# Kernel tuning notes

Measured on AMD Instinct MI355X. Metric: run time of the kernel, lower is better.

The kernel has to match this reference:

```python
import jax, jax.numpy as jnp
import numpy as np

S = 4096      # total packed sequence length (8 images x 512 patches)
D = 1152      # hidden_dim
H = 16        # num_heads
HD = D // H   # head_dim = 72
MLPD = 4304   # mlp_dim
EPS = 1e-5


def setup_inputs() -> dict:
    key = jax.random.key(0)
    ks = jax.random.split(key, 16)
    f32 = jnp.float32
    w = lambda k, shp: (jax.random.normal(k, shp, f32) * 0.02)
    hidden_states = jax.random.normal(ks[0], (S, D), f32)
    cu_seqlens = (jnp.arange(9, dtype=jnp.int32) * (S // 8))  # [0,512,...,4096]
    angles = jax.random.uniform(ks[1], (S, HD // 2), f32, 0.0, 2.0 * np.pi)
    rope_cos = jnp.cos(angles)
    rope_sin = jnp.sin(angles)
    return {
        "hidden_states": hidden_states,
        "cu_seqlens": cu_seqlens,
        "rope_cos": rope_cos,
        "rope_sin": rope_sin,
        "norm0_scale": jnp.ones((D,), f32),
        "norm0_bias": jnp.zeros((D,), f32),
        "wqkv_w": w(ks[2], (D, 3 * D)),
        "wqkv_b": jnp.zeros((3 * D,), f32),
        "wo_w": w(ks[3], (D, D)),
        "wo_b": jnp.zeros((D,), f32),
        "norm1_scale": jnp.ones((D,), f32),
        "norm1_bias": jnp.zeros((D,), f32),
        "fc0_w": w(ks[4], (D, MLPD)),
        "fc0_b": jnp.zeros((MLPD,), f32),
        "fc1_w": w(ks[5], (MLPD, D)),
        "fc1_b": jnp.zeros((D,), f32),
    }


def _layernorm(x, scale, bias):
    m = jnp.mean(x, axis=-1, keepdims=True)
    v = jnp.mean(jnp.square(x - m), axis=-1, keepdims=True)
    return (x - m) * jax.lax.rsqrt(v + EPS) * scale + bias


def _rope(x, cos, sin):
    # x: (S, H, HD). Complex multiply (x0 + i x1) * (cos + i sin) in real form.
    xr = x.reshape(S, H, HD // 2, 2)
    x0, x1 = xr[..., 0], xr[..., 1]
    c = cos[:, None, :]  # (S, 1, HD/2) broadcast over heads
    s = sin[:, None, :]
    o0 = x0 * c - x1 * s
    o1 = x0 * s + x1 * c
    return jnp.stack([o0, o1], axis=-1).reshape(S, H, HD)


def _block_diag_bias(cu_seqlens):
    positions = jnp.arange(S)
    starts, ends = cu_seqlens[:-1], cu_seqlens[1:]
    in_seg = (positions[:, None] >= starts[None, :]) & (positions[:, None] < ends[None, :])
    seg = jnp.argmax(in_seg.astype(jnp.int32), axis=-1)  # (S,)
    same = seg[:, None] == seg[None, :]
    return jnp.where(same, 0.0, jnp.finfo(jnp.float32).min)  # (S, S)


def reference(hidden_states, cu_seqlens, rope_cos, rope_sin,
              norm0_scale, norm0_bias, wqkv_w, wqkv_b, wo_w, wo_b,
              norm1_scale, norm1_bias, fc0_w, fc0_b, fc1_w, fc1_b):
    # pre-norm attention block
    x = _layernorm(hidden_states, norm0_scale, norm0_bias)
    qkv = (x @ wqkv_w + wqkv_b).reshape(S, 3, H, HD)
    q, k, v = qkv[:, 0], qkv[:, 1], qkv[:, 2]
    q = _rope(q, rope_cos, rope_sin)
    k = _rope(k, rope_cos, rope_sin)
    bias = _block_diag_bias(cu_seqlens)  # (S, S)
    scale = HD ** -0.5
    scores = jnp.einsum('shd,thd->hst', q, k) * scale + bias[None, :, :]
    probs = jax.nn.softmax(scores, axis=-1)
    attn = jnp.einsum('hst,thd->shd', probs, v).reshape(S, D)
    attn = attn @ wo_w + wo_b
    h = hidden_states + attn
    # pre-norm MLP block
    y = _layernorm(h, norm1_scale, norm1_bias)
    y = jax.nn.gelu(y @ fc0_w + fc0_b) @ fc1_w + fc1_b
    return h + y
```

## Files before the change

kernel.cpp:

```cpp
#include <hip/hip_runtime.h>


#define DEV __device__ __forceinline__

typedef __attribute__((ext_vector_type(8))) short short8;
typedef __attribute__((ext_vector_type(4))) float f32x4;

typedef const void __attribute__((address_space(1))) gvoid;
typedef void __attribute__((address_space(3))) lvoid;

DEV ushort f2bf(float f) {
  union { float f; unsigned u; } x; x.f = f;
  unsigned r = (x.u + 0x7FFFu + ((x.u >> 16) & 1u)) >> 16;
  return (ushort)r;
}

DEV float bf2f(ushort u) {
  union { unsigned u; float f; } x; x.u = (unsigned)u << 16;
  return x.f;
}

DEV void gload_lds16(const void* g, void* l) {
  __builtin_amdgcn_global_load_lds((gvoid*)g, (lvoid*)l, 16, 0, 0);
}

DEV f32x4 mfma16(short8 a, short8 b, f32x4 c) {
  return __builtin_amdgcn_mfma_f32_16x16x32_bf16(a, b, c, 0, 0, 0);
}

DEV float gelu_tanh(float x) {
  float x3 = x * x * x;
  return 0.5f * x * (1.f + tanhf(0.7978845608f * (x + 0.044715f * x3)));
}

__global__ void wconv_t(const float* __restrict__ src, ushort* __restrict__ dst,
                        int K, int N, int NP, int KP) {
  __shared__ float tile[32][33];
  const int k0 = blockIdx.x * 32, n0 = blockIdx.y * 32;
  const int tx = threadIdx.x & 31, ty = threadIdx.x >> 5;
#pragma unroll
  for (int i = 0; i < 4; ++i) {
    int r = ty + i * 8;
    float v = 0.f;
    if (k0 + r < K && n0 + tx < N) v = src[(size_t)(k0 + r) * N + n0 + tx];
    tile[tx][r] = v;
  }
  __syncthreads();
#pragma unroll
  for (int i = 0; i < 4; ++i) {
    int r = ty + i * 8;
    dst[(size_t)(n0 + r) * KP + k0 + tx] = f2bf(tile[r][tx]);
  }
}

__global__ __launch_bounds__(256) void ln_bf16(const float* __restrict__ x,
                                               const float* __restrict__ sc,
                                               const float* __restrict__ bi,
                                               ushort* __restrict__ out) {
  const int row = blockIdx.x, tid = threadIdx.x;
  const float* xr = x + (size_t)row * 1152;
  const int n = (tid < 128) ? 5 : 4;
  float vals[5];
  float s = 0.f, s2 = 0.f;
#pragma unroll
  for (int i = 0; i < 5; ++i) {
    if (i < n) { float v = xr[tid + i * 256]; vals[i] = v; s += v; s2 += v * v; }
  }
#pragma unroll
  for (int off = 32; off; off >>= 1) { s += __shfl_xor(s, off); s2 += __shfl_xor(s2, off); }
  __shared__ float rs[4], rs2[4];
  if ((tid & 63) == 0) { rs[tid >> 6] = s; rs2[tid >> 6] = s2; }
  __syncthreads();
  s = rs[0] + rs[1] + rs[2] + rs[3];
  s2 = rs2[0] + rs2[1] + rs2[2] + rs2[3];
  const float mean = s * (1.f / 1152.f);
  const float var = s2 * (1.f / 1152.f) - mean * mean;
  const float rstd = rsqrtf(var + 1e-5f);
  ushort* orow = out + (size_t)row * 1152;
  for (int i = 0; i < n; ++i) {
    int c = tid + i * 256;
    orow[c] = f2bf((vals[i] - mean) * rstd * sc[c] + bi[c]);
  }
}

template <int EPI>
__global__ __launch_bounds__(512, 2) void gemm_p(
    const ushort* __restrict__ A, const ushort* __restrict__ Bt,
    const float* __restrict__ bias, const float* __restrict__ resid,
    float* __restrict__ outf, ushort* __restrict__ outh,
    int N, int Kstride, int NT, int n_valid) {
  __shared__ ushort L[3][24576];
  const int tid = threadIdx.x;
  const int lane = tid & 63, wave = tid >> 6;
  const int l15 = lane & 15, lg = lane >> 4;

  const int nx = gridDim.x, ny = gridDim.y;
  const int nwg = nx * ny * gridDim.z;
  int flat = (blockIdx.z * ny + blockIdx.y) * nx + blockIdx.x;
  flat = (flat & 7) * (nwg >> 3) + (flat >> 3);
  const int bx = flat % nx;
  const int rem = flat / nx;
  const int by = rem % ny;
  const int bz = rem / ny;
  const int m0 = by * 256, n0 = bx * 128;
  const int k0 = bz * NT * 64;

  const int swz = ((tid & 7) ^ ((tid >> 3) & 7)) * 8;
  const int rstg = tid >> 3;
  const ushort* Ag = A + (size_t)(m0 + rstg) * Kstride + k0 + swz;
  const ushort* Bg = Bt + (size_t)(n0 + rstg) * Kstride + k0 + swz;

  auto stage = [&](int b, int t) {
    ushort* d = &L[b][0];
#pragma unroll
    for (int i = 0; i < 4; ++i)
      gload_lds16(Ag + ((size_t)i * 64) * Kstride + t * 64,
                  d + (i * 512 + wave * 64) * 8);
#pragma unroll
    for (int i = 0; i < 2; ++i)
      gload_lds16(Bg + ((size_t)i * 64) * Kstride + t * 64,
                  d + 16384 + (i * 512 + wave * 64) * 8);
  };

  const int wm = (wave >> 1) * 64, wn = (wave & 1) * 64;
  const int cph0 = (lg ^ (l15 & 7)) * 8;
  const int cph1 = ((4 + lg) ^ (l15 & 7)) * 8;

  auto rdfrag = [&](int b, short8 (&fa)[4][2], short8 (&fb)[4][2]) {
    const ushort* la = &L[b][0];
    const ushort* lb = &L[b][16384];
#pragma unroll
    for (int mf = 0; mf < 4; ++mf) {
      fa[mf][0] = *(const short8*)&la[(wm + mf * 16 + l15) * 64 + cph0];
      fa[mf][1] = *(const short8*)&la[(wm + mf * 16 + l15) * 64 + cph1];
    }
#pragma unroll
    for (int nf = 0; nf < 4; ++nf) {
      fb[nf][0] = *(const short8*)&lb[(wn + nf * 16 + l15) * 64 + cph0];
      fb[nf][1] = *(const short8*)&lb[(wn + nf * 16 + l15) * 64 + cph1];
    }
  };

  f32x4 acc[4][4] = {};
  short8 fa[2][4][2], fb[2][4][2];

  stage(0, 0); stage(1, 1); stage(2, 2);
  asm volatile("s_waitcnt vmcnt(6)" ::: "memory");
  __builtin_amdgcn_s_barrier();
  rdfrag(0, fa[0], fb[0]);

  int b0 = 0, b1 = 1;

#define GBODY(TT, CUR, NXT)                                                   \
  {                                                                           \
    const int _t = (TT);                                                      \
    if (_t + 1 < NT) rdfrag(b1, fa[NXT], fb[NXT]);                            \
    if (_t + 3 < NT) stage(b0, _t + 3);                                       \
    __builtin_amdgcn_s_setprio(1);                                            \
    _Pragma("unroll") for (int mf = 0; mf < 4; ++mf)                          \
      _Pragma("unroll") for (int nf = 0; nf < 4; ++nf) {                      \
        acc[mf][nf] = mfma16(fa[CUR][mf][0], fb[CUR][nf][0], acc[mf][nf]);    \
        acc[mf][nf] = mfma16(fa[CUR][mf][1], fb[CUR][nf][1], acc[mf][nf]);    \
      }                                                                       \
    __builtin_amdgcn_s_setprio(0);                                            \
    asm volatile("s_waitcnt lgkmcnt(0)" ::: "memory");                        \
    __builtin_amdgcn_sched_barrier(0);                                        \
    if (_t + 3 < NT) { asm volatile("s_waitcnt vmcnt(6)" ::: "memory"); }     \
    else if (_t + 2 < NT) { asm volatile("s_waitcnt vmcnt(0)" ::: "memory"); }\
    if (_t + 1 < NT) __builtin_amdgcn_s_barrier();                            \
    const int _b2 = 3 - b0 - b1; b0 = b1; b1 = _b2;                           \
  }

  for (int t = 0; t < NT; t += 2) {
    GBODY(t, 0, 1);
    GBODY(t + 1, 1, 0);
  }
#undef GBODY

  float* outp = outf;
  if constexpr (EPI == 0) outp = outf + (size_t)bz * ((size_t)4096 * N);
  const int cb = n0 + wn + l15;
  const int rb = m0 + wm + lg * 4;
#pragma unroll
  for (int j = 0; j < 4; ++j) {
    const int col = cb + j * 16;
    const float bv = (EPI != 0 && col < n_valid) ? bias[col] : 0.f;
#pragma unroll
    for (int i = 0; i < 4; ++i) {
#pragma unroll
      for (int r = 0; r < 4; ++r) {
        const int row = rb + i * 16 + r;
        const size_t idx = (size_t)row * N + col;
        const float v = acc[i][j][r] + bv;
        if constexpr (EPI == 0) outp[idx] = v;
        else if constexpr (EPI == 1) outf[idx] = resid[idx] + v;
        else if constexpr (EPI == 2) outh[idx] = f2bf(gelu_tanh(v));
        else outh[idx] = f2bf(v);
      }
    }
  }
}

__global__ __launch_bounds__(256) void ksum_reduce(
    const float* __restrict__ hb, const float* __restrict__ bias,
    const float* __restrict__ p0, const float* __restrict__ p1,
    float* __restrict__ out) {
  const f32x4* hb4 = (const f32x4*)hb;
  const f32x4* b4 = (const f32x4*)bias;
  const f32x4* p04 = (const f32x4*)p0;
  const f32x4* p14 = (const f32x4*)p1;
  f32x4* o4 = (f32x4*)out;
  const int total = 4096 * 288;
  for (int i = blockIdx.x * 256 + threadIdx.x; i < total; i += gridDim.x * 256) {
    f32x4 r = hb4[i] + b4[i % 288] + p04[i] + p14[i];
    o4[i] = r;
  }
}

__global__ void rope_pack(const ushort* __restrict__ qkv,
                          const float* __restrict__ cosp, const float* __restrict__ sinp,
                          ushort* __restrict__ qp, ushort* __restrict__ kp) {
  const int t = blockIdx.x * 256 + threadIdx.x;
  const int d = t % 96;
  const int hs = t / 96;
  const int h = hs & 15;
  const int s = hs >> 4;
  const size_t dst = ((size_t)h * 4096 + s) * 96 + d;
  if (d >= 72) { qp[dst] = 0; kp[dst] = 0; return; }
  const int i = d >> 1;
  const float c = cosp[s * 36 + i], sn = sinp[s * 36 + i];
  const size_t base = (size_t)s * 3456 + h * 72;
  const float q0 = bf2f(qkv[base + (d & ~1)]), q1 = bf2f(qkv[base + (d | 1)]);
  const float k0 = bf2f(qkv[base + 1152 + (d & ~1)]), k1 = bf2f(qkv[base + 1152 + (d | 1)]);
  float qo, ko;
  if ((d & 1) == 0) { qo = q0 * c - q1 * sn; ko = k0 * c - k1 * sn; }
  else              { qo = q0 * sn + q1 * c; ko = k0 * sn + k1 * c; }
  qp[dst] = f2bf(qo * 0.1178511302f);
  kp[dst] = f2bf(ko);
}

__global__ void v_pack(const ushort* __restrict__ qkv, ushort* __restrict__ vt) {
  __shared__ ushort lv[96][64];
  const int b = blockIdx.x;
  const int h = b >> 6;
  const int s0 = (b & 63) << 6;
  const int tid = threadIdx.x;
#pragma unroll
  for (int it = 0; it < 24; ++it) {
    int idx = tid + it * 256;
    int d = idx % 96, sl = idx / 96;
    lv[d][sl] = (d < 72) ? qkv[(size_t)(s0 + sl) * 3456 + 2304 + h * 72 + d] : (ushort)0;
  }
  __syncthreads();
#pragma unroll
  for (int it = 0; it < 24; ++it) {
    int idx = tid + it * 256;
    int d = idx >> 6, sl = idx & 63;
    vt[((size_t)h * 96 + d) * 4096 + s0 + sl] = lv[d][sl];
  }
}

__global__ __launch_bounds__(256) void attn_kernel(
    const ushort* __restrict__ qp, const ushort* __restrict__ kp,
    const ushort* __restrict__ vt, ushort* __restrict__ attn_out) {
  __shared__ ushort lp[4][16 * 32];
  const int tid = threadIdx.x, lane = tid & 63, wave = tid >> 6;
  const int l15 = lane & 15, lg = lane >> 4;
  const int b = blockIdx.x;
  const int h = b >> 6;
  const int rem = b & 63;
  const int seg = rem >> 3, qt = rem & 7;
  const int q0 = seg * 512 + qt * 64 + wave * 16;

  short8 aq[3];
  const ushort* qrow = qp + ((size_t)h * 4096 + q0 + l15) * 96 + lg * 8;
  aq[0] = *(const short8*)(qrow);
  aq[1] = *(const short8*)(qrow + 32);
  aq[2] = *(const short8*)(qrow + 64);

  f32x4 oacc[5] = {};
  float mrow[4] = {-1e30f, -1e30f, -1e30f, -1e30f};
  float srow[4] = {0.f, 0.f, 0.f, 0.f};

  const ushort* kbase = kp + ((size_t)h * 4096 + seg * 512) * 96;
  const ushort* vbase = vt + (size_t)h * 96 * 4096 + seg * 512;
  ushort* lpw = lp[wave];

  for (int kc = 0; kc < 16; ++kc) {
    f32x4 sc[2] = {};
#pragma unroll
    for (int n = 0; n < 2; ++n) {
      const ushort* krow = kbase + (size_t)(kc * 32 + n * 16 + l15) * 96 + lg * 8;
#pragma unroll
      for (int c = 0; c < 3; ++c) {
        short8 kb = *(const short8*)(krow + c * 32);
        sc[n] = mfma16(aq[c], kb, sc[n]);
      }
    }
    float corr[4];
#pragma unroll
    for (int j = 0; j < 4; ++j) {
      float v = fmaxf(sc[0][j], sc[1][j]);
      v = fmaxf(v, __shfl_xor(v, 1));
      v = fmaxf(v, __shfl_xor(v, 2));
      v = fmaxf(v, __shfl_xor(v, 4));
      v = fmaxf(v, __shfl_xor(v, 8));
      float mn = fmaxf(mrow[j], v);
      corr[j] = __expf(mrow[j] - mn);
      mrow[j] = mn;
    }
    float p0[4], p1[4];
#pragma unroll
    for (int j = 0; j < 4; ++j) {
      p0[j] = __expf(sc[0][j] - mrow[j]);
      p1[j] = __expf(sc[1][j] - mrow[j]);
      float ps = p0[j] + p1[j];
      ps += __shfl_xor(ps, 1);
      ps += __shfl_xor(ps, 2);
      ps += __shfl_xor(ps, 4);
      ps += __shfl_xor(ps, 8);
      srow[j] = srow[j] * corr[j] + ps;
    }
#pragma unroll
    for (int n = 0; n < 5; ++n)
#pragma unroll
      for (int j = 0; j < 4; ++j)
        oacc[n][j] *= corr[j];
#pragma unroll
    for (int j = 0; j < 4; ++j) {
      int row = lg * 4 + j;
      lpw[row * 32 + l15] = f2bf(p0[j]);
      lpw[row * 32 + 16 + l15] = f2bf(p1[j]);
    }
    __syncthreads();
    short8 pa = *(const short8*)&lpw[l15 * 32 + lg * 8];
    const ushort* vrow = vbase + kc * 32 + lg * 8;
#pragma unroll
    for (int n = 0; n < 5; ++n) {
      short8 vb = *(const short8*)(vrow + (size_t)(n * 16 + l15) * 4096);
      oacc[n] = mfma16(pa, vb, oacc[n]);
    }
    __syncthreads();
  }
#pragma unroll
  for (int j = 0; j < 4; ++j) {
    float inv = 1.f / srow[j];
    int row = q0 + lg * 4 + j;
#pragma unroll
    for (int n = 0; n < 5; ++n) {
      int col = n * 16 + l15;
      if (col < 72)
        attn_out[(size_t)row * 1152 + h * 72 + col] = f2bf(oacc[n][j] * inv);
    }
  }
}

extern "C" void kernel_launch(void* const* d_in, const int* in_sizes, int n_in,
                              void* d_out, int out_size, void* d_ws, size_t ws_size,
                              hipStream_t stream) {
  (void)in_sizes; (void)n_in; (void)out_size;
  const float* hidden = (const float*)d_in[0];
  const float* ropec = (const float*)d_in[2];
  const float* ropes = (const float*)d_in[3];
  const float* n0s = (const float*)d_in[4];
  const float* n0b = (const float*)d_in[5];
  const float* wqkv = (const float*)d_in[6];
  const float* bqkv = (const float*)d_in[7];
  const float* wo = (const float*)d_in[8];
  const float* bo = (const float*)d_in[9];
  const float* n1s = (const float*)d_in[10];
  const float* n1b = (const float*)d_in[11];
  const float* wfc0 = (const float*)d_in[12];
  const float* bfc0 = (const float*)d_in[13];
  const float* wfc1 = (const float*)d_in[14];
  const float* bfc1 = (const float*)d_in[15];
  float* out = (float*)d_out;

  char* ws = (char*)d_ws;
  ushort* x_bf   = (ushort*)(ws + 0);
  ushort* wqkv_t = (ushort*)(ws + 9437184);
  ushort* wo_t   = (ushort*)(ws + 17399808);
  ushort* fc0_t  = (ushort*)(ws + 20054016);
  ushort* fc1_t  = (ushort*)(ws + 30081024);
  ushort* qkv_bf = (ushort*)(ws + 40108032);
  ushort* mid    = (ushort*)(ws + 40108032);
  ushort* q_pad  = (ushort*)(ws + 96731136);
  ushort* k_pad  = (ushort*)(ws + 109314048);
  ushort* vt     = (ushort*)(ws + 121896960);
  float*  pbuf   = (float*)(ws + 96731136);
  ushort* attn   = (ushort*)(ws + 134479872);
  float*  hbuf   = (float*)(ws + 143917056);
  ushort* yln    = (ushort*)(ws + 162791424);
  if (ws_size < 172228608) return;

  wconv_t<<<dim3(36, 108), 256, 0, stream>>>(wqkv, wqkv_t, 1152, 3456, 3456, 1152);
  wconv_t<<<dim3(36, 36), 256, 0, stream>>>(wo, wo_t, 1152, 1152, 1152, 1152);
  wconv_t<<<dim3(36, 136), 256, 0, stream>>>(wfc0, fc0_t, 1152, 4304, 4352, 1152);
  wconv_t<<<dim3(136, 36), 256, 0, stream>>>(wfc1, fc1_t, 4304, 1152, 1152, 4352);

  ln_bf16<<<4096, 256, 0, stream>>>(hidden, n0s, n0b, x_bf);

  gemm_p<3><<<dim3(27, 16), 512, 0, stream>>>(x_bf, wqkv_t, bqkv, nullptr, nullptr, qkv_bf,
                                              3456, 1152, 18, 3456);
  rope_pack<<<24576, 256, 0, stream>>>(qkv_bf, ropec, ropes, q_pad, k_pad);
  v_pack<<<1024, 256, 0, stream>>>(qkv_bf, vt);

  attn_kernel<<<1024, 256, 0, stream>>>(q_pad, k_pad, vt, attn);

  gemm_p<1><<<dim3(9, 16), 512, 0, stream>>>(attn, wo_t, bo, hidden, hbuf, nullptr,
                                             1152, 1152, 18, 1152);
  ln_bf16<<<4096, 256, 0, stream>>>(hbuf, n1s, n1b, yln);

  gemm_p<2><<<dim3(34, 16), 512, 0, stream>>>(yln, fc0_t, bfc0, nullptr, nullptr, mid,
                                              4352, 1152, 18, 4304);
  gemm_p<0><<<dim3(9, 16, 2), 512, 0, stream>>>(mid, fc1_t, nullptr, nullptr, pbuf, nullptr,
                                                1152, 4352, 34, 1152);
  ksum_reduce<<<2048, 256, 0, stream>>>(hbuf, bfc1, pbuf, pbuf + (size_t)4096 * 1152, out);
}
```

Before: 378.3 us.

## Use 256x256 GEMM tiles with fine-grained quarter-step pipeline and vectorize rope_pack

The GEMM kernel moves from 256x128 to 256x256 output tiles with double-buffered LDS. Each k-step is split into four MFMA quarters, interleaved with staged global-to-LDS loads and fragment reads under explicit barriers. Weight buffers are padded to multiples of 256 columns to fit the new tile width, and the grid dimensions and workspace layout are updated to match. rope_pack is also vectorized to process 8 elements per thread with 16-byte loads and stores. The larger tile halves B traffic per output, but it uses more accumulator registers and fewer workgroups, which hurts tile quantization on the 1152-wide GEMMs.

```diff
diff --git a/kernel.cpp b/kernel.cpp
--- a/kernel.cpp
+++ b/kernel.cpp
@@ -83,16 +83,36 @@
   }
 }
 
+#define BAR __builtin_amdgcn_s_barrier()
+#define LGKM0 do { asm volatile("s_waitcnt lgkmcnt(0)" ::: "memory"); \
+                   __builtin_amdgcn_sched_barrier(0); } while (0)
+#define VM6 do { asm volatile("s_waitcnt vmcnt(6)" ::: "memory"); \
+                 __builtin_amdgcn_sched_barrier(0); } while (0)
+#define MMQ(AF, BF, MB, NB)                                                   \
+  do {                                                                        \
+    __builtin_amdgcn_s_setprio(1);                                            \
+    _Pragma("unroll") for (int mf = 0; mf < 4; ++mf)                          \
+      _Pragma("unroll") for (int nf = 0; nf < 2; ++nf) {                      \
+        acc[(MB) + mf][(NB) + nf] =                                           \
+            mfma16(AF[mf][0], BF[nf][0], acc[(MB) + mf][(NB) + nf]);          \
+        acc[(MB) + mf][(NB) + nf] =                                           \
+            mfma16(AF[mf][1], BF[nf][1], acc[(MB) + mf][(NB) + nf]);          \
+      }                                                                       \
+    __builtin_amdgcn_s_setprio(0);                                            \
+  } while (0)
+
 template <int EPI>
-__global__ __launch_bounds__(512, 2) void gemm_p(
+__global__ __launch_bounds__(512, 2) void gemmT(
     const ushort* __restrict__ A, const ushort* __restrict__ Bt,
     const float* __restrict__ bias, const float* __restrict__ resid,
     float* __restrict__ outf, ushort* __restrict__ outh,
-    int N, int Kstride, int NT, int n_valid) {
-  __shared__ ushort L[3][24576];
+    int N, int K, int NT, int n_valid) {
+  __shared__ ushort lA[2][256 * 64];
+  __shared__ ushort lB[2][256 * 64];
   const int tid = threadIdx.x;
   const int lane = tid & 63, wave = tid >> 6;
   const int l15 = lane & 15, lg = lane >> 4;
+  const int wr = wave >> 2, wc = wave & 3;
 
   const int nx = gridDim.x, ny = gridDim.y;
   const int nwg = nx * ny * gridDim.z;
@@ -102,96 +122,99 @@
   const int rem = flat / nx;
   const int by = rem % ny;
   const int bz = rem / ny;
-  const int m0 = by * 256, n0 = bx * 128;
+  const int m0 = by * 256, n0 = bx * 256;
   const int k0 = bz * NT * 64;
 
-  const int swz = ((tid & 7) ^ ((tid >> 3) & 7)) * 8;
-  const int rstg = tid >> 3;
-  const ushort* Ag = A + (size_t)(m0 + rstg) * Kstride + k0 + swz;
-  const ushort* Bg = Bt + (size_t)(n0 + rstg) * Kstride + k0 + swz;
-
-  auto stage = [&](int b, int t) {
-    ushort* d = &L[b][0];
-#pragma unroll
-    for (int i = 0; i < 4; ++i)
-      gload_lds16(Ag + ((size_t)i * 64) * Kstride + t * 64,
-                  d + (i * 512 + wave * 64) * 8);
-#pragma unroll
-    for (int i = 0; i < 2; ++i)
-      gload_lds16(Bg + ((size_t)i * 64) * Kstride + t * 64,
-                  d + 16384 + (i * 512 + wave * 64) * 8);
+  const int rb8 = tid >> 3;
+  const int swz = ((tid & 7) ^ (rb8 & 7)) * 8;
+  const ushort* Ag = A + (size_t)m0 * K + k0 + swz;
+  const ushort* Bg = Bt + (size_t)n0 * K + k0 + swz;
+  const int rB = (rb8 & 31) + ((rb8 >> 5) << 6);
+  const int rBw = (wave & 3) * 8 + (wave >> 2) * 64;
+
+  auto stA = [&](int b, int u, int t) {
+#pragma unroll
+    for (int j = 0; j < 2; ++j) {
+      const int r = u * 64 + rb8 + j * 128;
+      gload_lds16(Ag + (size_t)r * K + t * 64,
+                  &lA[b][(u * 64 + wave * 8 + j * 128) * 64]);
+    }
   };
-
-  const int wm = (wave >> 1) * 64, wn = (wave & 1) * 64;
-  const int cph0 = (lg ^ (l15 & 7)) * 8;
-  const int cph1 = ((4 + lg) ^ (l15 & 7)) * 8;
-
-  auto rdfrag = [&](int b, short8 (&fa)[4][2], short8 (&fb)[4][2]) {
-    const ushort* la = &L[b][0];
-    const ushort* lb = &L[b][16384];
+  auto stB = [&](int b, int c, int t) {
+#pragma unroll
+    for (int j = 0; j < 2; ++j) {
+      const int r = rB + c * 32 + j * 128;
+      gload_lds16(Bg + (size_t)r * K + t * 64,
+                  &lB[b][(rBw + c * 32 + j * 128) * 64]);
+    }
+  };
+
+  const int arow = wr * 128 + l15;
+  const int brow = wc * 64 + l15;
+  const int cp0 = ((0 + lg) ^ (l15 & 7)) * 8;
+  const int cp1 = ((4 + lg) ^ (l15 & 7)) * 8;
+  auto rdA = [&](int b, int half, short8 (&a)[4][2]) {
 #pragma unroll
     for (int mf = 0; mf < 4; ++mf) {
-      fa[mf][0] = *(const short8*)&la[(wm + mf * 16 + l15) * 64 + cph0];
-      fa[mf][1] = *(const short8*)&la[(wm + mf * 16 + l15) * 64 + cph1];
-    }
-#pragma unroll
-    for (int nf = 0; nf < 4; ++nf) {
-      fb[nf][0] = *(const short8*)&lb[(wn + nf * 16 + l15) * 64 + cph0];
-      fb[nf][1] = *(const short8*)&lb[(wn + nf * 16 + l15) * 64 + cph1];
+      const ushort* p = &lA[b][(arow + half * 64 + mf * 16) * 64];
+      a[mf][0] = *(const short8*)(p + cp0);
+      a[mf][1] = *(const short8*)(p + cp1);
     }
   };
-
-  f32x4 acc[4][4] = {};
-  short8 fa[2][4][2], fb[2][4][2];
-
-  stage(0, 0); stage(1, 1); stage(2, 2);
-  asm volatile("s_waitcnt vmcnt(6)" ::: "memory");
-  __builtin_amdgcn_s_barrier();
-  rdfrag(0, fa[0], fb[0]);
-
-  int b0 = 0, b1 = 1;
-
-#define GBODY(TT, CUR, NXT)                                                   \
-  {                                                                           \
-    const int _t = (TT);                                                      \
-    if (_t + 1 < NT) rdfrag(b1, fa[NXT], fb[NXT]);                            \
-    if (_t + 3 < NT) stage(b0, _t + 3);                                       \
-    __builtin_amdgcn_s_setprio(1);                                            \
-    _Pragma("unroll") for (int mf = 0; mf < 4; ++mf)                          \
-      _Pragma("unroll") for (int nf = 0; nf < 4; ++nf) {                      \
-        acc[mf][nf] = mfma16(fa[CUR][mf][0], fb[CUR][nf][0], acc[mf][nf]);    \
-        acc[mf][nf] = mfma16(fa[CUR][mf][1], fb[CUR][nf][1], acc[mf][nf]);    \
-      }                                                                       \
-    __builtin_amdgcn_s_setprio(0);                                            \
-    asm volatile("s_waitcnt lgkmcnt(0)" ::: "memory");                        \
-    __builtin_amdgcn_sched_barrier(0);                                        \
-    if (_t + 3 < NT) { asm volatile("s_waitcnt vmcnt(6)" ::: "memory"); }     \
-    else if (_t + 2 < NT) { asm volatile("s_waitcnt vmcnt(0)" ::: "memory"); }\
-    if (_t + 1 < NT) __builtin_amdgcn_s_barrier();                            \
-    const int _b2 = 3 - b0 - b1; b0 = b1; b1 = _b2;                           \
-  }
-
-  for (int t = 0; t < NT; t += 2) {
-    GBODY(t, 0, 1);
-    GBODY(t + 1, 1, 0);
-  }
-#undef GBODY
+  auto rdB = [&](int b, int h, short8 (&bb)[2][2]) {
+#pragma unroll
+    for (int nf = 0; nf < 2; ++nf) {
+      const ushort* p = &lB[b][(brow + h * 32 + nf * 16) * 64];
+      bb[nf][0] = *(const short8*)(p + cp0);
+      bb[nf][1] = *(const short8*)(p + cp1);
+    }
+  };
+
+  f32x4 acc[8][4] = {};
+  short8 aL[4][2], aH[4][2], b01[2][2], b23[2][2];
+
+  stA(0, 0, 0); stB(0, 0, 0); stA(0, 1, 0); stB(0, 1, 0);
+  stA(1, 0, 1); stB(1, 0, 1); stA(1, 1, 1); stB(1, 1, 1);
+  asm volatile("s_waitcnt vmcnt(8)" ::: "memory");
+  BAR;
+  rdA(0, 0, aL); rdB(0, 0, b01);
+
+  const int NIT = NT >> 1;
+  for (int it = 0; it < NIT; ++it) {
+    const int tn0 = 2 * it + 2, tn1 = 2 * it + 3;
+    const bool more = (it + 1 < NIT);
+    rdB(0, 1, b23); if (more) stA(0, 0, tn0);
+    BAR; LGKM0; MMQ(aL, b01, 0, 0); BAR;
+    rdA(0, 1, aH); if (more) stB(0, 0, tn0);
+    BAR; LGKM0; MMQ(aL, b23, 0, 2); BAR;
+    if (more) stA(0, 1, tn0);
+    BAR; LGKM0; MMQ(aH, b01, 4, 0); VM6; BAR;
+    rdA(1, 0, aL); rdB(1, 0, b01); if (more) stB(0, 1, tn0);
+    BAR; LGKM0; MMQ(aH, b23, 4, 2); BAR;
+    rdB(1, 1, b23); if (more) stA(1, 0, tn1);
+    BAR; LGKM0; MMQ(aL, b01, 0, 0); BAR;
+    rdA(1, 1, aH); if (more) stB(1, 0, tn1);
+    BAR; LGKM0; MMQ(aL, b23, 0, 2); BAR;
+    if (more) stA(1, 1, tn1);
+    BAR; LGKM0; MMQ(aH, b01, 4, 0); VM6; BAR;
+    rdA(0, 0, aL); rdB(0, 0, b01); if (more) stB(1, 1, tn1);
+    BAR; LGKM0; MMQ(aH, b23, 4, 2); BAR;
+  }
 
   float* outp = outf;
-  if constexpr (EPI == 0) outp = outf + (size_t)bz * ((size_t)4096 * N);
-  const int cb = n0 + wn + l15;
-  const int rb = m0 + wm + lg * 4;
-#pragma unroll
-  for (int j = 0; j < 4; ++j) {
-    const int col = cb + j * 16;
-    const float bv = (EPI != 0 && col < n_valid) ? bias[col] : 0.f;
-#pragma unroll
-    for (int i = 0; i < 4; ++i) {
+  if constexpr (EPI == 0) outp = outf + (size_t)bz * 4096 * 1152;
+#pragma unroll
+  for (int nf = 0; nf < 4; ++nf) {
+    const int col = n0 + wc * 64 + nf * 16 + l15;
+    if (col >= n_valid) continue;
+    const float bv = (EPI != 0) ? bias[col] : 0.f;
+#pragma unroll
+    for (int mf = 0; mf < 8; ++mf) {
 #pragma unroll
       for (int r = 0; r < 4; ++r) {
-        const int row = rb + i * 16 + r;
+        const int row = m0 + wr * 128 + mf * 16 + lg * 4 + r;
         const size_t idx = (size_t)row * N + col;
-        const float v = acc[i][j][r] + bv;
+        const float v = acc[mf][nf][r] + bv;
         if constexpr (EPI == 0) outp[idx] = v;
         else if constexpr (EPI == 1) outf[idx] = resid[idx] + v;
         else if constexpr (EPI == 2) outh[idx] = f2bf(gelu_tanh(v));
@@ -211,32 +234,43 @@
   const f32x4* p14 = (const f32x4*)p1;
   f32x4* o4 = (f32x4*)out;
   const int total = 4096 * 288;
-  for (int i = blockIdx.x * 256 + threadIdx.x; i < total; i += gridDim.x * 256) {
-    f32x4 r = hb4[i] + b4[i % 288] + p04[i] + p14[i];
-    o4[i] = r;
-  }
-}
-
-__global__ void rope_pack(const ushort* __restrict__ qkv,
-                          const float* __restrict__ cosp, const float* __restrict__ sinp,
-                          ushort* __restrict__ qp, ushort* __restrict__ kp) {
+  for (int i = blockIdx.x * 256 + threadIdx.x; i < total; i += gridDim.x * 256)
+    o4[i] = hb4[i] + b4[i % 288] + p04[i] + p14[i];
+}
+
+__global__ __launch_bounds__(256) void rope_pack(
+    const ushort* __restrict__ qkv,
+    const float* __restrict__ cosp, const float* __restrict__ sinp,
+    ushort* __restrict__ qp, ushort* __restrict__ kp) {
   const int t = blockIdx.x * 256 + threadIdx.x;
-  const int d = t % 96;
-  const int hs = t / 96;
+  const int c = t % 12;
+  const int hs = t / 12;
   const int h = hs & 15;
   const int s = hs >> 4;
-  const size_t dst = ((size_t)h * 4096 + s) * 96 + d;
-  if (d >= 72) { qp[dst] = 0; kp[dst] = 0; return; }
-  const int i = d >> 1;
-  const float c = cosp[s * 36 + i], sn = sinp[s * 36 + i];
-  const size_t base = (size_t)s * 3456 + h * 72;
-  const float q0 = bf2f(qkv[base + (d & ~1)]), q1 = bf2f(qkv[base + (d | 1)]);
-  const float k0 = bf2f(qkv[base + 1152 + (d & ~1)]), k1 = bf2f(qkv[base + 1152 + (d | 1)]);
-  float qo, ko;
-  if ((d & 1) == 0) { qo = q0 * c - q1 * sn; ko = k0 * c - k1 * sn; }
-  else              { qo = q0 * sn + q1 * c; ko = k0 * sn + k1 * c; }
-  qp[dst] = f2bf(qo * 0.1178511302f);
-  kp[dst] = f2bf(ko);
+  const size_t dst = ((size_t)h * 4096 + s) * 96 + c * 8;
+  if (c >= 9) {
+    short8 z = {};
+    *(short8*)(qp + dst) = z;
+    *(short8*)(kp + dst) = z;
+    return;
+  }
+  const size_t base = (size_t)s * 3456 + h * 72 + c * 8;
+  const short8 qv = *(const short8*)(qkv + base);
+  const short8 kv = *(const short8*)(qkv + base + 1152);
+  const f32x4 cs = *(const f32x4*)(cosp + s * 36 + c * 4);
+  const f32x4 sn = *(const f32x4*)(sinp + s * 36 + c * 4);
+  short8 qo, ko;
+#pragma unroll
+  for (int j = 0; j < 4; ++j) {
+    const float q0 = bf2f((ushort)qv[2 * j]), q1 = bf2f((ushort)qv[2 * j + 1]);
+    const float k0 = bf2f((ushort)kv[2 * j]), k1 = bf2f((ushort)kv[2 * j + 1]);
+    qo[2 * j] = (short)f2bf((q0 * cs[j] - q1 * sn[j]) * 0.1178511302f);
+    qo[2 * j + 1] = (short)f2bf((q0 * sn[j] + q1 * cs[j]) * 0.1178511302f);
+    ko[2 * j] = (short)f2bf(k0 * cs[j] - k1 * sn[j]);
+    ko[2 * j + 1] = (short)f2bf(k0 * sn[j] + k1 * cs[j]);
+  }
+  *(short8*)(qp + dst) = qo;
+  *(short8*)(kp + dst) = ko;
 }
 
 __global__ void v_pack(const ushort* __restrict__ qkv, ushort* __restrict__ vt) {
@@ -379,41 +413,41 @@
   char* ws = (char*)d_ws;
   ushort* x_bf   = (ushort*)(ws + 0);
   ushort* wqkv_t = (ushort*)(ws + 9437184);
-  ushort* wo_t   = (ushort*)(ws + 17399808);
-  ushort* fc0_t  = (ushort*)(ws + 20054016);
-  ushort* fc1_t  = (ushort*)(ws + 30081024);
-  ushort* qkv_bf = (ushort*)(ws + 40108032);
-  ushort* mid    = (ushort*)(ws + 40108032);
-  ushort* q_pad  = (ushort*)(ws + 96731136);
-  ushort* k_pad  = (ushort*)(ws + 109314048);
-  ushort* vt     = (ushort*)(ws + 121896960);
-  float*  pbuf   = (float*)(ws + 96731136);
-  ushort* attn   = (ushort*)(ws + 134479872);
-  float*  hbuf   = (float*)(ws + 143917056);
-  ushort* yln    = (ushort*)(ws + 162791424);
-  if (ws_size < 172228608) return;
-
-  wconv_t<<<dim3(36, 108), 256, 0, stream>>>(wqkv, wqkv_t, 1152, 3456, 3456, 1152);
-  wconv_t<<<dim3(36, 36), 256, 0, stream>>>(wo, wo_t, 1152, 1152, 1152, 1152);
+  ushort* wo_t   = (ushort*)(ws + 17694720);
+  ushort* fc0_t  = (ushort*)(ws + 20643840);
+  ushort* fc1_t  = (ushort*)(ws + 30670848);
+  ushort* qkv_bf = (ushort*)(ws + 41811968);
+  ushort* mid    = (ushort*)(ws + 41811968);
+  ushort* q_pad  = (ushort*)(ws + 77463552);
+  ushort* k_pad  = (ushort*)(ws + 90046464);
+  ushort* vt     = (ushort*)(ws + 102629376);
+  float*  pbuf   = (float*)(ws + 77463552);
+  ushort* attn   = (ushort*)(ws + 115212288);
+  float*  hbuf   = (float*)(ws + 124649472);
+  ushort* yln    = (ushort*)(ws + 143523840);
+  if (ws_size < 152961024) return;
+
+  wconv_t<<<dim3(36, 112), 256, 0, stream>>>(wqkv, wqkv_t, 1152, 3456, 3584, 1152);
+  wconv_t<<<dim3(36, 40), 256, 0, stream>>>(wo, wo_t, 1152, 1152, 1280, 1152);
   wconv_t<<<dim3(36, 136), 256, 0, stream>>>(wfc0, fc0_t, 1152, 4304, 4352, 1152);
-  wconv_t<<<dim3(136, 36), 256, 0, stream>>>(wfc1, fc1_t, 4304, 1152, 1152, 4352);
+  wconv_t<<<dim3(136, 40), 256, 0, stream>>>(wfc1, fc1_t, 4304, 1152, 1280, 4352);
 
   ln_bf16<<<4096, 256, 0, stream>>>(hidden, n0s, n0b, x_bf);
 
-  gemm_p<3><<<dim3(27, 16), 512, 0, stream>>>(x_bf, wqkv_t, bqkv, nullptr, nullptr, qkv_bf,
-                                              3456, 1152, 18, 3456);
-  rope_pack<<<24576, 256, 0, stream>>>(qkv_bf, ropec, ropes, q_pad, k_pad);
+  gemmT<3><<<dim3(14, 16), 512, 0, stream>>>(x_bf, wqkv_t, bqkv, nullptr, nullptr, qkv_bf,
+                                             3456, 1152, 18, 3456);
+  rope_pack<<<3072, 256, 0, stream>>>(qkv_bf, ropec, ropes, q_pad, k_pad);
   v_pack<<<1024, 256, 0, stream>>>(qkv_bf, vt);
 
   attn_kernel<<<1024, 256, 0, stream>>>(q_pad, k_pad, vt, attn);
 
-  gemm_p<1><<<dim3(9, 16), 512, 0, stream>>>(attn, wo_t, bo, hidden, hbuf, nullptr,
-                                             1152, 1152, 18, 1152);
+  gemmT<1><<<dim3(5, 16), 512, 0, stream>>>(attn, wo_t, bo, hidden, hbuf, nullptr,
+                                            1152, 1152, 18, 1152);
   ln_bf16<<<4096, 256, 0, stream>>>(hbuf, n1s, n1b, yln);
 
-  gemm_p<2><<<dim3(34, 16), 512, 0, stream>>>(yln, fc0_t, bfc0, nullptr, nullptr, mid,
-                                              4352, 1152, 18, 4304);
-  gemm_p<0><<<dim3(9, 16, 2), 512, 0, stream>>>(mid, fc1_t, nullptr, nullptr, pbuf, nullptr,
-                                                1152, 4352, 34, 1152);
+  gemmT<2><<<dim3(17, 16), 512, 0, stream>>>(yln, fc0_t, bfc0, nullptr, nullptr, mid,
+                                             4352, 1152, 18, 4304);
+  gemmT<0><<<dim3(5, 16, 2), 512, 0, stream>>>(mid, fc1_t, nullptr, nullptr, pbuf, nullptr,
+                                               1152, 4352, 34, 1152);
   ksum_reduce<<<2048, 256, 0, stream>>>(hbuf, bfc1, pbuf, pbuf + (size_t)4096 * 1152, out);
 }
```

After: 401.3 us. 6.1% more time.
